# Optimization experiments

Measured on AMD Instinct MI355X. Metric: run time of the kernel, lower is better.

Reference implementation:

```python
import jax, jax.numpy as jnp
import numpy as np

B, N, IN_DIM = 16, 2048, 64
DIM, HEADS, DEPTH, K, NCLS = 512, 8, 4, 256, 2
DH = DIM // HEADS
EPS = 1e-5


def layernorm(h, s, b):
    mu = jnp.mean(h, axis=-1, keepdims=True)
    var = jnp.mean(jnp.square(h - mu), axis=-1, keepdims=True)
    return (h - mu) * jax.lax.rsqrt(var + EPS) * s + b


def setup_inputs() -> dict:
    key = jax.random.key(0)
    ks = jax.random.split(key, 20)
    w = 0.02
    L = DEPTH
    return {
        "x": jax.random.normal(ks[0], (B, N, IN_DIM), jnp.float32),
        "emb_w": jax.random.normal(ks[1], (IN_DIM, DIM), jnp.float32) * w,
        "emb_b": jnp.zeros((DIM,), jnp.float32),
        "pos": jax.random.normal(ks[2], (1, N, DIM), jnp.float32) * w,
        "ln1_s": jnp.ones((L, DIM), jnp.float32),
        "ln1_b": jnp.zeros((L, DIM), jnp.float32),
        "wq": jax.random.normal(ks[3], (L, DIM, DIM), jnp.float32) * w,
        "wk": jax.random.normal(ks[4], (L, DIM, DIM), jnp.float32) * w,
        "wv": jax.random.normal(ks[5], (L, DIM, DIM), jnp.float32) * w,
        "pk": jax.random.normal(ks[6], (L, N, K), jnp.float32) * (1.0 / np.sqrt(N)),
        "pv": jax.random.normal(ks[7], (L, N, K), jnp.float32) * (1.0 / np.sqrt(N)),
        "wo": jax.random.normal(ks[8], (L, DIM, DIM), jnp.float32) * w,
        "wo_b": jnp.zeros((L, DIM), jnp.float32),
        "ln2_s": jnp.ones((L, DIM), jnp.float32),
        "ln2_b": jnp.zeros((L, DIM), jnp.float32),
        "w1": jax.random.normal(ks[9], (L, DIM, 4 * DIM), jnp.float32) * w,
        "b1": jnp.zeros((L, 4 * DIM), jnp.float32),
        "w2": jax.random.normal(ks[10], (L, 4 * DIM, DIM), jnp.float32) * w,
        "b2": jnp.zeros((L, DIM), jnp.float32),
        "fc_w": jax.random.normal(ks[11], (DIM, NCLS), jnp.float32) * w,
        "fc_b": jnp.zeros((NCLS,), jnp.float32),
    }


def reference(x, emb_w, emb_b, pos, ln1_s, ln1_b, wq, wk, wv, pk, pv, wo, wo_b,
              ln2_s, ln2_b, w1, b1, w2, b2, fc_w, fc_b):
    scale = DH ** -0.5
    h = x @ emb_w + emb_b + pos  # [B,N,DIM]
    for i in range(DEPTH):
        # Linformer self-attention (PreNorm + residual)
        z = layernorm(h, ln1_s[i], ln1_b[i])
        q = (z @ wq[i]).reshape(B, N, HEADS, DH)
        k = z @ wk[i]  # [B,N,DIM]
        v = z @ wv[i]
        # low-rank projection along sequence: [B,N,DIM] x [N,K] -> [B,K,DIM]
        kp = jnp.einsum('bnd,nk->bkd', k, pk[i]).reshape(B, K, HEADS, DH)
        vp = jnp.einsum('bnd,nk->bkd', v, pv[i]).reshape(B, K, HEADS, DH)
        dots = jnp.einsum('bnhd,bkhd->bhnk', q, kp) * scale
        attn = jax.nn.softmax(dots, axis=-1)
        out = jnp.einsum('bhnk,bkhd->bnhd', attn, vp).reshape(B, N, DIM)
        h = h + out @ wo[i] + wo_b[i]
        # FeedForward (PreNorm + residual)
        z = layernorm(h, ln2_s[i], ln2_b[i])
        h = h + jax.nn.gelu(z @ w1[i] + b1[i]) @ w2[i] + b2[i]
    pooled = jnp.mean(h, axis=1)  # [B,DIM]
    return pooled @ fc_w + fc_b  # [B,NCLS]
```

## Files before the change

### kernel.cpp

```cpp
#include <hip/hip_runtime.h>
#include <math.h>

#define B_    16
#define N_    2048
#define INDIM 64
#define DIM_  512
#define HEADS 8
#define DEPTH 4
#define KLIN  256
#define NCLS  2
#define DH    64
#define EPSF  1e-5f

typedef __attribute__((ext_vector_type(8))) short short8v;
typedef __attribute__((ext_vector_type(4))) short short4v;
typedef __attribute__((ext_vector_type(4))) float f32x4;

#define SBAR() __builtin_amdgcn_sched_barrier(0)

__device__ __forceinline__ short f2bf(float f) {
  unsigned u = __float_as_uint(f);
  u += 0x7FFFu + ((u >> 16) & 1u);
  return (short)(u >> 16);
}

__device__ __forceinline__ float wave_sum(float v) {
  #pragma unroll
  for (int o = 32; o > 0; o >>= 1) v += __shfl_xor(v, o);
  return v;
}

__device__ __forceinline__ float gelu_tanh(float x) {
  float u = x * (1.5957691216057308f + 0.07135481627f * x * x);
  return x / (1.f + __expf(-u));
}

__device__ __forceinline__ void gl_lds16(const short* g, short* l) {
  __builtin_amdgcn_global_load_lds(
      (const __attribute__((address_space(1))) unsigned int*)g,
      (__attribute__((address_space(3))) unsigned int*)l, 16, 0, 0);
}

__global__ __launch_bounds__(256) void tconv_k(const float* __restrict__ src,
                                               short* __restrict__ dst, int R,
                                               int C, long long sSrc,
                                               long long sDst) {
  __shared__ float tile[32][33];
  int c0 = blockIdx.x * 32, r0 = blockIdx.y * 32;
  src += (long long)blockIdx.z * sSrc;
  dst += (long long)blockIdx.z * sDst;
  int tx = threadIdx.x & 31, ty = threadIdx.x >> 5;
  #pragma unroll
  for (int rr = 0; rr < 4; ++rr)
    tile[ty + rr * 8][tx] = src[(long long)(r0 + ty + rr * 8) * C + c0 + tx];
  __syncthreads();
  #pragma unroll
  for (int rr = 0; rr < 4; ++rr) {
    int c = ty + rr * 8;
    dst[(long long)(c0 + c) * R + r0 + tx] = f2bf(tile[tx][c]);
  }
}

__global__ __launch_bounds__(256) void cconv_k(const float* __restrict__ src,
                                               short* __restrict__ dst,
                                               int n8) {
  int i = blockIdx.x * 256 + threadIdx.x;
  if (i < n8) {
    const float* s = src + (long long)i * 8;
    float4 a = *(const float4*)s, c = *(const float4*)(s + 4);
    short8v o = {f2bf(a.x), f2bf(a.y), f2bf(a.z), f2bf(a.w),
                 f2bf(c.x), f2bf(c.y), f2bf(c.z), f2bf(c.w)};
    *(short8v*)(dst + (long long)i * 8) = o;
  }
}

__global__ __launch_bounds__(256) void tpose_k(const short* __restrict__ src,
                                               short* __restrict__ dst, int R,
                                               int C, long long sSrc,
                                               long long sDst) {
  __shared__ __align__(16) short tile[64][72];
  int c0 = blockIdx.x * 64, r0 = blockIdx.y * 64;
  src += (long long)blockIdx.z * sSrc;
  dst += (long long)blockIdx.z * sDst;
  int t = threadIdx.x;
  #pragma unroll
  for (int rep = 0; rep < 2; ++rep) {
    int row = rep * 32 + (t >> 3), c8 = (t & 7) * 8;
    *(short8v*)&tile[row][c8] =
        *(const short8v*)(src + (long long)(r0 + row) * C + c0 + c8);
  }
  __syncthreads();
  #pragma unroll
  for (int rep = 0; rep < 2; ++rep) {
    int c = rep * 32 + (t >> 3), r8 = (t & 7) * 8;
    short8v o;
    #pragma unroll
    for (int j = 0; j < 8; ++j) o[j] = tile[r8 + j][c];
    *(short8v*)(dst + (long long)(c0 + c) * R + r0 + r8) = o;
  }
}

__global__ __launch_bounds__(256) void ln_k(const float* __restrict__ h,
                                            const float* __restrict__ s,
                                            const float* __restrict__ b,
                                            short* __restrict__ z) {
  int lane = threadIdx.x & 63;
  long long row = ((long long)blockIdx.x << 2) + (threadIdx.x >> 6);
  const float* hr = h + row * DIM_ + lane * 8;
  float4 a = *(const float4*)hr;
  float4 c = *(const float4*)(hr + 4);
  float sum = a.x + a.y + a.z + a.w + c.x + c.y + c.z + c.w;
  sum = wave_sum(sum);
  float mu = sum * (1.f / DIM_);
  float d[8] = {a.x - mu, a.y - mu, a.z - mu, a.w - mu,
                c.x - mu, c.y - mu, c.z - mu, c.w - mu};
  float vs = 0.f;
  #pragma unroll
  for (int i = 0; i < 8; ++i) vs += d[i] * d[i];
  vs = wave_sum(vs);
  float rstd = rsqrtf(vs * (1.f / DIM_) + EPSF);
  const float* sp = s + lane * 8;
  const float* bp = b + lane * 8;
  float4 s0 = *(const float4*)sp, s1 = *(const float4*)(sp + 4);
  float4 b0 = *(const float4*)bp, b1 = *(const float4*)(bp + 4);
  float o[8];
  o[0] = d[0] * rstd * s0.x + b0.x; o[1] = d[1] * rstd * s0.y + b0.y;
  o[2] = d[2] * rstd * s0.z + b0.z; o[3] = d[3] * rstd * s0.w + b0.w;
  o[4] = d[4] * rstd * s1.x + b1.x; o[5] = d[5] * rstd * s1.y + b1.y;
  o[6] = d[6] * rstd * s1.z + b1.z; o[7] = d[7] * rstd * s1.w + b1.w;
  short8v ov = {f2bf(o[0]), f2bf(o[1]), f2bf(o[2]), f2bf(o[3]),
                f2bf(o[4]), f2bf(o[5]), f2bf(o[6]), f2bf(o[7])};
  *(short8v*)(z + row * DIM_ + lane * 8) = ov;
}

template <int OUTBF, int BM, int BN>
__global__ __launch_bounds__(256) void gemm_bf(
    const short* __restrict__ A, const short* __restrict__ Bsrc,
    const float* __restrict__ bias, const float* __restrict__ resid,
    void* __restrict__ Cv, int M, int N, int K, int lda, int ldb, int ldc,
    long long sAb, long long sBb, long long sCb, int dualThresh,
    long long dualOff, int epi, int resMod) {
  constexpr int MT = BM / 32;
  constexpr int NT = BN / 32;
  constexpr int NLD = BM / 32 + BN / 32;
  int zz = blockIdx.z;
  A += (long long)zz * sAb;
  Bsrc += (long long)zz * sBb;
  int bm = blockIdx.y * BM, bn = blockIdx.x * BN;
  if (dualThresh && bm >= dualThresh) Bsrc += dualOff;
  int t = threadIdx.x;
  __shared__ __align__(16) short Alds[2][BM * 64];
  __shared__ __align__(16) short Blds[2][BN * 64];
  int lane = t & 63, wid = t >> 6;
  int lr = lane & 15, q = lane >> 4;
  int wm = (wid >> 1) * (BM / 2), wn = (wid & 1) * (BN / 2);
  int rl = lane >> 3;
  int cs = (lane & 7) ^ rl;
  f32x4 acc[MT][NT] = {};

  auto stage = [&](int buf, int k0) {
    #pragma unroll
    for (int i = 0; i < BM / 32; ++i) {
      int rb = i * 32 + wid * 8;
      gl_lds16(A + (long long)(bm + rb + rl) * lda + k0 + cs * 8,
               &Alds[buf][rb * 64]);
    }
    #pragma unroll
    for (int i = 0; i < BN / 32; ++i) {
      int rb = i * 32 + wid * 8;
      gl_lds16(Bsrc + (long long)(bn + rb + rl) * ldb + k0 + cs * 8,
               &Blds[buf][rb * 64]);
    }
  };

  stage(0, 0);
  int cur = 0;
  for (int k0 = 0; k0 < K; k0 += 64, cur ^= 1) {
    if (k0 + 64 < K) {
      stage(cur ^ 1, k0 + 64);
      SBAR();
      asm volatile("s_waitcnt vmcnt(%0)" ::"n"(NLD) : "memory");
    } else {
      SBAR();
      asm volatile("s_waitcnt vmcnt(0)" ::: "memory");
    }
    __builtin_amdgcn_s_barrier();
    SBAR();
    #pragma unroll
    for (int kk2 = 0; kk2 < 2; ++kk2) {
      short8v af[MT], bfr[NT];
      #pragma unroll
      for (int mi = 0; mi < MT; ++mi)
        af[mi] = *(const short8v*)&Alds[cur][(wm + mi * 16 + lr) * 64 +
                                             (((kk2 << 2) | q) ^ (lr & 7)) * 8];
      #pragma unroll
      for (int ni = 0; ni < NT; ++ni)
        bfr[ni] = *(const short8v*)&Blds[cur][(wn + ni * 16 + lr) * 64 +
                                              (((kk2 << 2) | q) ^ (lr & 7)) * 8];
      #pragma unroll
      for (int mi = 0; mi < MT; ++mi)
        #pragma unroll
        for (int ni = 0; ni < NT; ++ni)
          acc[mi][ni] = __builtin_amdgcn_mfma_f32_16x16x32_bf16(
              bfr[ni], af[mi], acc[mi][ni], 0, 0, 0);
    }
    SBAR();
    __builtin_amdgcn_s_barrier();
  }

  #pragma unroll
  for (int mi = 0; mi < MT; ++mi) {
    int m = bm + wm + mi * 16 + lr;
    int rm = (epi == 2 && resMod) ? (m % resMod) : m;
    #pragma unroll
    for (int ni = 0; ni < NT; ++ni) {
      int nb = bn + wn + ni * 16 + q * 4;
      f32x4 v = acc[mi][ni];
      if (epi >= 1) {
        float4 bb = *(const float4*)(bias + nb);
        v[0] += bb.x; v[1] += bb.y; v[2] += bb.z; v[3] += bb.w;
      }
      if (epi == 2) {
        float4 rr = *(const float4*)(resid + (long long)rm * ldc + nb);
        v[0] += rr.x; v[1] += rr.y; v[2] += rr.z; v[3] += rr.w;
      } else if (epi == 3) {
        v[0] = gelu_tanh(v[0]); v[1] = gelu_tanh(v[1]);
        v[2] = gelu_tanh(v[2]); v[3] = gelu_tanh(v[3]);
      }
      long long base = (long long)zz * sCb + (long long)m * ldc + nb;
      if (OUTBF) {
        short4v o = {f2bf(v[0]), f2bf(v[1]), f2bf(v[2]), f2bf(v[3])};
        *(short4v*)((short*)Cv + base) = o;
      } else {
        *(float4*)((float*)Cv + base) = make_float4(v[0], v[1], v[2], v[3]);
      }
    }
  }
}

template <int OUTBF, int BM, int BN, int EPI>
__global__ __launch_bounds__(512, 2) void gemm8(
    const short* __restrict__ A, const short* __restrict__ Bt,
    const float* __restrict__ bias, const float* __restrict__ resid,
    void* __restrict__ Cv, int M, int N, int K, long long sAb, long long sBb,
    long long sCb, int dualThresh, long long dualOff) {
  constexpr int MH = BM / 64;
  constexpr int WCOL = BN / 4;
  constexpr int NT = WCOL / 16;
  constexpr int NTH = NT / 2;
  constexpr int LB = BN / 128;
  constexpr int LA = BM / 128;
  __shared__ __align__(16) short Alds[2][BM * 64];
  __shared__ __align__(16) short Blds[2][BN * 64];
  const int tid = threadIdx.x;
  const int lane = tid & 63, wid = tid >> 6;
  const int lr = lane & 15, q = lane >> 4;
  const int wm = (wid >> 2) * (BM / 2), wn = (wid & 3) * WCOL;
  const int rl = lane >> 3, cs = (lane & 7) ^ rl;
  const int zz = blockIdx.z;
  A += (long long)zz * sAb;
  Bt += (long long)zz * sBb;
  const int nwg = gridDim.x * gridDim.y;
  int bid = blockIdx.y * gridDim.x + blockIdx.x;
  const int nx8 = nwg >> 3, r8 = nwg & 7, xcd = bid & 7, loc = bid >> 3;
  int swz = (xcd < r8 ? xcd * (nx8 + 1) : r8 * (nx8 + 1) + (xcd - r8) * nx8)
            + loc;
  const int bm = (swz / gridDim.x) * BM, bn = (swz % gridDim.x) * BN;
  if (dualThresh && bm >= dualThresh) Bt += dualOff;
  const short* Ag = A + (long long)bm * K + cs * 8;
  const short* Bg = Bt + (long long)bn * K + cs * 8;
  f32x4 acc[2 * MH][NT] = {};

  auto stageA = [&](int slot, int h, int k0) {
    #pragma unroll
    for (int j = 0; j < LA; ++j) {
      int rb = h * (BM / 2) + j * 64 + wid * 8;
      gl_lds16(Ag + (long long)(rb + rl) * K + k0, &Alds[slot][rb * 64]);
    }
  };
  auto stageB = [&](int slot, int h, int k0) {
    #pragma unroll
    for (int j = 0; j < LB; ++j) {
      int rb = h * (BN / 2) + j * 64 + wid * 8;
      gl_lds16(Bg + (long long)(rb + rl) * K + k0, &Blds[slot][rb * 64]);
    }
  };
  auto rd = [&](const short* Ls, int row, int kk) -> short8v {
    return *(const short8v*)&Ls[row * 64 + ((((kk << 2) | q) ^ (lr & 7)) << 3)];
  };
  auto mfma4 = [&](short8v (&af)[MH][2], short8v (&bf)[NTH][2], int mo,
                   int no) {
    #pragma unroll
    for (int mi = 0; mi < MH; ++mi)
      #pragma unroll
      for (int ni = 0; ni < NTH; ++ni)
        #pragma unroll
        for (int kk = 0; kk < 2; ++kk)
          acc[mo + mi][no + ni] = __builtin_amdgcn_mfma_f32_16x16x32_bf16(
              bf[ni][kk], af[mi][kk], acc[mo + mi][no + ni], 0, 0, 0);
  };

  const int T = K >> 6;
  stageA(0, 0, 0); stageA(0, 1, 0); stageB(0, 0, 0); stageB(0, 1, 0);
  if (T > 1) {
    stageA(1, 0, 64);
    SBAR();
    asm volatile("s_waitcnt vmcnt(%0)" ::"n"(LA) : "memory");
  } else {
    SBAR();
    asm volatile("s_waitcnt vmcnt(0)" ::: "memory");
  }
  __builtin_amdgcn_s_barrier();

  for (int tt = 0; tt < T; ++tt) {
    const int s = tt & 1, ns = s ^ 1;
    const int kn = (tt + 1) << 6, kn2 = (tt + 2) << 6;
    const short* Als = Alds[s];
    const short* Bls = Blds[s];
    short8v af0[MH][2], af1[MH][2], bf0[NTH][2], bf1[NTH][2];
    SBAR();
    #pragma unroll
    for (int mi = 0; mi < MH; ++mi)
      #pragma unroll
      for (int kk = 0; kk < 2; ++kk)
        af0[mi][kk] = rd(Als, wm + mi * 16 + lr, kk);
    #pragma unroll
    for (int ni = 0; ni < NTH; ++ni)
      #pragma unroll
      for (int kk = 0; kk < 2; ++kk)
        bf0[ni][kk] = rd(Bls, wn + ni * 16 + lr, kk);
    if (tt + 1 < T) stageA(ns, 1, kn);
    if (BN == 256) asm volatile("s_waitcnt lgkmcnt(8)" ::: "memory");
    SBAR();
    __builtin_amdgcn_s_barrier();
    asm volatile("s_waitcnt lgkmcnt(0)" ::: "memory");
    SBAR();
    __builtin_amdgcn_s_setprio(1);
    mfma4(af0, bf0, 0, 0);
    __builtin_amdgcn_s_setprio(0);
    SBAR();
    __builtin_amdgcn_s_barrier();
    SBAR();
    #pragma unroll
    for (int ni = 0; ni < NTH; ++ni)
      #pragma unroll
      for (int kk = 0; kk < 2; ++kk)
        bf1[ni][kk] = rd(Bls, wn + (NTH + ni) * 16 + lr, kk);
    SBAR();
    __builtin_amdgcn_s_barrier();
    asm volatile("s_waitcnt lgkmcnt(0)" ::: "memory");
    SBAR();
    __builtin_amdgcn_s_setprio(1);
    mfma4(af0, bf1, 0, NTH);
    __builtin_amdgcn_s_setprio(0);
    SBAR();
    __builtin_amdgcn_s_barrier();
    SBAR();
    #pragma unroll
    for (int mi = 0; mi < MH; ++mi)
      #pragma unroll
      for (int kk = 0; kk < 2; ++kk)
        af1[mi][kk] = rd(Als, wm + MH * 16 + mi * 16 + lr, kk);
    if (tt + 1 < T) { stageB(ns, 0, kn); stageB(ns, 1, kn); }
    SBAR();
    __builtin_amdgcn_s_barrier();
    asm volatile("s_waitcnt lgkmcnt(0)" ::: "memory");
    SBAR();
    __builtin_amdgcn_s_setprio(1);
    mfma4(af1, bf0, MH, 0);
    __builtin_amdgcn_s_setprio(0);
    SBAR();
    __builtin_amdgcn_s_barrier();
    SBAR();
    if (tt + 2 < T) stageA(s, 0, kn2);
    SBAR();
    __builtin_amdgcn_s_barrier();
    __builtin_amdgcn_s_setprio(1);
    mfma4(af1, bf1, MH, NTH);
    __builtin_amdgcn_s_setprio(0);
    if (tt + 2 < T) {
      SBAR();
      asm volatile("s_waitcnt vmcnt(%0)" ::"n"(LA) : "memory");
    } else if (tt + 1 < T) {
      SBAR();
      asm volatile("s_waitcnt vmcnt(0)" ::: "memory");
    }
    SBAR();
    __builtin_amdgcn_s_barrier();
  }

  #pragma unroll
  for (int mi = 0; mi < 2 * MH; ++mi) {
    int m = bm + wm + mi * 16 + lr;
    #pragma unroll
    for (int nj = 0; nj < NT; ++nj) {
      int nb = bn + wn + nj * 16 + q * 4;
      f32x4 v = acc[mi][nj];
      if (EPI >= 1) {
        float4 bb = *(const float4*)(bias + nb);
        v[0] += bb.x; v[1] += bb.y; v[2] += bb.z; v[3] += bb.w;
      }
      if (EPI == 2) {
        float4 rr = *(const float4*)(resid + (long long)m * N + nb);
        v[0] += rr.x; v[1] += rr.y; v[2] += rr.z; v[3] += rr.w;
      } else if (EPI == 3) {
        v[0] = gelu_tanh(v[0]); v[1] = gelu_tanh(v[1]);
        v[2] = gelu_tanh(v[2]); v[3] = gelu_tanh(v[3]);
      }
      long long base = (long long)zz * sCb + (long long)m * N + nb;
      if (OUTBF) {
        short4v o = {f2bf(v[0]), f2bf(v[1]), f2bf(v[2]), f2bf(v[3])};
        *(short4v*)((short*)Cv + base) = o;
      } else {
        *(float4*)((float*)Cv + base) = make_float4(v[0], v[1], v[2], v[3]);
      }
    }
  }
}

template <int OUTBF, int BM, int BN, int EPI>
__global__ __launch_bounds__(512, 2) void gemm8m(
    const short* __restrict__ A, const short* __restrict__ Bt,
    const float* __restrict__ bias, const float* __restrict__ resid,
    void* __restrict__ Cv, int M, int N, int K, long long sAb, long long sBb,
    long long sCb, int dualThresh, long long dualOff) {
  constexpr int MH = BM / 64;
  constexpr int WCOL = BN / 4;
  constexpr int NT = WCOL / 16;
  constexpr int NTH = NT / 2;
  constexpr int LB = BN / 128;
  constexpr int LA = BM / 128;
  __shared__ __align__(16) short Alds[2][BM * 64];
  __shared__ __align__(16) short Blds[2][BN * 64];
  const int tid = threadIdx.x;
  const int lane = tid & 63, wid = tid >> 6;
  const int lr = lane & 15, q = lane >> 4;
  const int wm = (wid >> 2) * (BM / 2), wn = (wid & 3) * WCOL;
  const int rl = lane >> 3, cs = (lane & 7) ^ rl;
  const int zz = blockIdx.z;
  A += (long long)zz * sAb;
  Bt += (long long)zz * sBb;
  const int nwg = gridDim.x * gridDim.y;
  int bid = blockIdx.y * gridDim.x + blockIdx.x;
  const int nx8 = nwg >> 3, r8 = nwg & 7, xcd = bid & 7, loc = bid >> 3;
  int swz = (xcd < r8 ? xcd * (nx8 + 1) : r8 * (nx8 + 1) + (xcd - r8) * nx8)
            + loc;
  const int bm = (swz / gridDim.x) * BM, bn = (swz % gridDim.x) * BN;
  if (dualThresh && bm >= dualThresh) Bt += dualOff;
  const short* Ag = A + (long long)bm * K + cs * 8;
  const short* Bg = Bt + (long long)bn * K + cs * 8;
  f32x4 acc[2 * MH][NT] = {};

  auto stageA = [&](int slot, int h, int k0) {
    #pragma unroll
    for (int j = 0; j < LA; ++j) {
      int rb = h * (BM / 2) + j * 64 + wid * 8;
      gl_lds16(Ag + (long long)(rb + rl) * K + k0, &Alds[slot][rb * 64]);
    }
  };
  auto stageB = [&](int slot, int h, int k0) {
    #pragma unroll
    for (int j = 0; j < LB; ++j) {
      int rb = h * (BN / 2) + j * 64 + wid * 8;
      gl_lds16(Bg + (long long)(rb + rl) * K + k0, &Blds[slot][rb * 64]);
    }
  };
  auto rd = [&](const short* Ls, int row, int kk) -> short8v {
    return *(const short8v*)&Ls[row * 64 + ((((kk << 2) | q) ^ (lr & 7)) << 3)];
  };
  auto mfma4 = [&](short8v (&af)[MH][2], short8v (&bf)[NTH][2], int mo,
                   int no) {
    #pragma unroll
    for (int mi = 0; mi < MH; ++mi)
      #pragma unroll
      for (int ni = 0; ni < NTH; ++ni)
        #pragma unroll
        for (int kk = 0; kk < 2; ++kk)
          acc[mo + mi][no + ni] = __builtin_amdgcn_mfma_f32_16x16x32_bf16(
              bf[ni][kk], af[mi][kk], acc[mo + mi][no + ni], 0, 0, 0);
  };

  const int T = K >> 6;
  stageA(0, 0, 0); stageA(0, 1, 0); stageB(0, 0, 0); stageB(0, 1, 0);
  if (T > 1) {
    stageA(1, 0, 64);
    SBAR();
    asm volatile("s_waitcnt vmcnt(%0)" ::"n"(LA) : "memory");
  } else {
    SBAR();
    asm volatile("s_waitcnt vmcnt(0)" ::: "memory");
  }
  __builtin_amdgcn_s_barrier();

  for (int tt = 0; tt < T; ++tt) {
    const int s = tt & 1, ns = s ^ 1;
    const int kn = (tt + 1) << 6, kn2 = (tt + 2) << 6;
    const short* Als = Alds[s];
    const short* Bls = Blds[s];
    short8v af0[MH][2], af1[MH][2], bf0[NTH][2], bf1[NTH][2];
    SBAR();
    #pragma unroll
    for (int mi = 0; mi < MH; ++mi)
      #pragma unroll
      for (int kk = 0; kk < 2; ++kk)
        af0[mi][kk] = rd(Als, wm + mi * 16 + lr, kk);
    #pragma unroll
    for (int ni = 0; ni < NTH; ++ni)
      #pragma unroll
      for (int kk = 0; kk < 2; ++kk) {
        bf0[ni][kk] = rd(Bls, wn + ni * 16 + lr, kk);
        bf1[ni][kk] = rd(Bls, wn + (NTH + ni) * 16 + lr, kk);
      }
    if (tt + 1 < T) {
      stageA(ns, 1, kn);
      stageB(ns, 0, kn);
      stageB(ns, 1, kn);
    }
    SBAR();
    __builtin_amdgcn_s_barrier();
    asm volatile("s_waitcnt lgkmcnt(0)" ::: "memory");
    SBAR();
    __builtin_amdgcn_s_setprio(1);
    mfma4(af0, bf0, 0, 0);
    mfma4(af0, bf1, 0, NTH);
    __builtin_amdgcn_s_setprio(0);
    SBAR();
    __builtin_amdgcn_s_barrier();
    SBAR();
    #pragma unroll
    for (int mi = 0; mi < MH; ++mi)
      #pragma unroll
      for (int kk = 0; kk < 2; ++kk)
        af1[mi][kk] = rd(Als, wm + MH * 16 + mi * 16 + lr, kk);
    if (tt + 2 < T) stageA(s, 0, kn2);
    SBAR();
    __builtin_amdgcn_s_barrier();
    asm volatile("s_waitcnt lgkmcnt(0)" ::: "memory");
    SBAR();
    __builtin_amdgcn_s_setprio(1);
    mfma4(af1, bf0, MH, 0);
    mfma4(af1, bf1, MH, NTH);
    __builtin_amdgcn_s_setprio(0);
    if (tt + 2 < T) {
      SBAR();
      asm volatile("s_waitcnt vmcnt(%0)" ::"n"(LA) : "memory");
    } else if (tt + 1 < T) {
      SBAR();
      asm volatile("s_waitcnt vmcnt(0)" ::: "memory");
    }
    SBAR();
    __builtin_amdgcn_s_barrier();
  }

  #pragma unroll
  for (int mi = 0; mi < 2 * MH; ++mi) {
    int m = bm + wm + mi * 16 + lr;
    #pragma unroll
    for (int nj = 0; nj < NT; ++nj) {
      int nb = bn + wn + nj * 16 + q * 4;
      f32x4 v = acc[mi][nj];
      if (EPI >= 1) {
        float4 bb = *(const float4*)(bias + nb);
        v[0] += bb.x; v[1] += bb.y; v[2] += bb.z; v[3] += bb.w;
      }
      if (EPI == 2) {
        float4 rr = *(const float4*)(resid + (long long)m * N + nb);
        v[0] += rr.x; v[1] += rr.y; v[2] += rr.z; v[3] += rr.w;
      } else if (EPI == 3) {
        v[0] = gelu_tanh(v[0]); v[1] = gelu_tanh(v[1]);
        v[2] = gelu_tanh(v[2]); v[3] = gelu_tanh(v[3]);
      }
      long long base = (long long)zz * sCb + (long long)m * N + nb;
      if (OUTBF) {
        short4v o = {f2bf(v[0]), f2bf(v[1]), f2bf(v[2]), f2bf(v[3])};
        *(short4v*)((short*)Cv + base) = o;
      } else {
        *(float4*)((float*)Cv + base) = make_float4(v[0], v[1], v[2], v[3]);
      }
    }
  }
}

__global__ __launch_bounds__(256) void attn_k(short* __restrict__ qc,
                                              const short* __restrict__ kvp,
                                              const short* __restrict__ vt,
                                              float scale) {
  int n0 = blockIdx.x * 64, hh = blockIdx.y, b = blockIdx.z;
  int t = threadIdx.x;
  int lane = t & 63, w = t >> 6;
  int lr = lane & 15, qd = lane >> 4;

  __shared__ __align__(16) short Qlds[64][72];
  __shared__ __align__(16) short Kbuf[256 * 72];
  __shared__ __align__(16) short Vt[64][264];
  auto Klds = (short(*)[72])Kbuf;
  auto Plds = (short(*)[264])Kbuf;

  short* qptr = qc + (long long)b * N_ * DIM_ + hh * DH;
  const short* kptr = kvp + (long long)b * 2 * KLIN * DIM_ + hh * DH;
  const short* vtp = vt + (long long)b * DIM_ * KLIN + (long long)hh * DH * KLIN;

  #pragma unroll
  for (int rep = 0; rep < 2; ++rep) {
    int L = rep * 256 + t, row = L >> 3, c8 = (L & 7) << 3;
    *(short8v*)&Qlds[row][c8] =
        *(const short8v*)(qptr + (long long)(n0 + row) * DIM_ + c8);
  }
  #pragma unroll
  for (int rep = 0; rep < 8; ++rep) {
    int L = rep * 256 + t, row = L >> 3, c8 = (L & 7) << 3;
    *(short8v*)&Klds[row][c8] =
        *(const short8v*)(kptr + (long long)row * DIM_ + c8);
  }
  #pragma unroll
  for (int rep = 0; rep < 8; ++rep) {
    int L = rep * 256 + t, row = L >> 5, c8 = (L & 31) << 3;
    *(short8v*)&Vt[row][c8] =
        *(const short8v*)(vtp + (long long)row * KLIN + c8);
  }
  __syncthreads();

  short8v qa0 = *(const short8v*)&Qlds[16 * w + lr][qd * 8];
  short8v qa1 = *(const short8v*)&Qlds[16 * w + lr][32 + qd * 8];
  f32x4 sacc[16];
  #pragma unroll
  for (int nt = 0; nt < 16; ++nt) {
    short8v b0 = *(const short8v*)&Klds[nt * 16 + lr][qd * 8];
    short8v b1 = *(const short8v*)&Klds[nt * 16 + lr][32 + qd * 8];
    f32x4 acc = {};
    acc = __builtin_amdgcn_mfma_f32_16x16x32_bf16(b0, qa0, acc, 0, 0, 0);
    acc = __builtin_amdgcn_mfma_f32_16x16x32_bf16(b1, qa1, acc, 0, 0, 0);
    sacc[nt] = acc;
  }

  float mx = -1e30f;
  #pragma unroll
  for (int nt = 0; nt < 16; ++nt)
    #pragma unroll
    for (int r = 0; r < 4; ++r) mx = fmaxf(mx, sacc[nt][r]);
  mx = fmaxf(mx, __shfl_xor(mx, 16));
  mx = fmaxf(mx, __shfl_xor(mx, 32));
  float rs = 0.f;
  #pragma unroll
  for (int nt = 0; nt < 16; ++nt)
    #pragma unroll
    for (int r = 0; r < 4; ++r) {
      float e = __expf((sacc[nt][r] - mx) * scale);
      sacc[nt][r] = e;
      rs += e;
    }
  rs += __shfl_xor(rs, 16);
  rs += __shfl_xor(rs, 32);
  float inv = 1.f / rs;

  __syncthreads();
  #pragma unroll
  for (int nt = 0; nt < 16; ++nt) {
    short4v p = {f2bf(sacc[nt][0] * inv), f2bf(sacc[nt][1] * inv),
                 f2bf(sacc[nt][2] * inv), f2bf(sacc[nt][3] * inv)};
    *(short4v*)&Plds[16 * w + lr][nt * 16 + qd * 4] = p;
  }
  __syncthreads();

  f32x4 out[4] = {};
  #pragma unroll
  for (int k0 = 0; k0 < 8; ++k0) {
    short8v ap = *(const short8v*)&Plds[16 * w + lr][k0 * 32 + qd * 8];
    #pragma unroll
    for (int n2 = 0; n2 < 4; ++n2) {
      short8v bv = *(const short8v*)&Vt[n2 * 16 + lr][k0 * 32 + qd * 8];
      out[n2] =
          __builtin_amdgcn_mfma_f32_16x16x32_bf16(bv, ap, out[n2], 0, 0, 0);
    }
  }

  long long rowoff = (long long)(n0 + 16 * w + lr) * DIM_;
  #pragma unroll
  for (int n2 = 0; n2 < 4; ++n2) {
    short4v o = {f2bf(out[n2][0]), f2bf(out[n2][1]), f2bf(out[n2][2]),
                 f2bf(out[n2][3])};
    *(short4v*)(qptr + rowoff + n2 * 16 + qd * 4) = o;
  }
}

__global__ __launch_bounds__(256) void pool1_k(const float* __restrict__ h,
                                               float* __restrict__ partial) {
  int stripe = blockIdx.x, b = blockIdx.y;
  int c4 = (threadIdx.x & 127) * 4, half = threadIdx.x >> 7;
  const float* base =
      h + ((long long)b * N_ + stripe * 128 + half * 64) * DIM_ + c4;
  float4 acc = {0.f, 0.f, 0.f, 0.f};
  for (int r = 0; r < 64; ++r) {
    float4 v = *(const float4*)(base + (long long)r * DIM_);
    acc.x += v.x; acc.y += v.y; acc.z += v.z; acc.w += v.w;
  }
  __shared__ float red[512];
  if (half == 1) *(float4*)&red[c4] = acc;
  __syncthreads();
  if (half == 0) {
    float4 o = *(const float4*)&red[c4];
    o.x += acc.x; o.y += acc.y; o.z += acc.z; o.w += acc.w;
    *(float4*)&partial[((long long)b * 16 + stripe) * DIM_ + c4] = o;
  }
}
__global__ __launch_bounds__(256) void pool2_k(const float* __restrict__ partial,
                                               float* __restrict__ pooled) {
  int b = blockIdx.x;
  for (int c = threadIdx.x; c < DIM_; c += 256) {
    float s = 0.f;
    for (int k = 0; k < 16; ++k) s += partial[((long long)b * 16 + k) * DIM_ + c];
    pooled[b * DIM_ + c] = s * (1.f / N_);
  }
}

__global__ __launch_bounds__(64) void fc_k(const float* __restrict__ pooled,
                                           const float* __restrict__ fc_w,
                                           const float* __restrict__ fc_b,
                                           float* __restrict__ out) {
  int t = threadIdx.x;
  if (t < B_ * NCLS) {
    int b = t >> 1, c = t & 1;
    float s = fc_b[c];
    for (int d = 0; d < DIM_; ++d)
      s += pooled[b * DIM_ + d] * fc_w[d * NCLS + c];
    out[t] = s;
  }
}

extern "C" void kernel_launch(void* const* d_in, const int* in_sizes, int n_in,
                              void* d_out, int out_size, void* d_ws,
                              size_t ws_size, hipStream_t stream) {
  const float* x     = (const float*)d_in[0];
  const float* emb_w = (const float*)d_in[1];
  const float* emb_b = (const float*)d_in[2];
  const float* pos   = (const float*)d_in[3];
  const float* ln1_s = (const float*)d_in[4];
  const float* ln1_b = (const float*)d_in[5];
  const float* wq    = (const float*)d_in[6];
  const float* wk    = (const float*)d_in[7];
  const float* wv    = (const float*)d_in[8];
  const float* pk    = (const float*)d_in[9];
  const float* pv    = (const float*)d_in[10];
  const float* wo    = (const float*)d_in[11];
  const float* wo_b  = (const float*)d_in[12];
  const float* ln2_s = (const float*)d_in[13];
  const float* ln2_b = (const float*)d_in[14];
  const float* w1    = (const float*)d_in[15];
  const float* b1    = (const float*)d_in[16];
  const float* w2    = (const float*)d_in[17];
  const float* b2    = (const float*)d_in[18];
  const float* fc_w  = (const float*)d_in[19];
  const float* fc_b  = (const float*)d_in[20];
  float* out = (float*)d_out;

  const bool big = ws_size >= (size_t)230 * 1024 * 1024;
  const int acb = big ? 16 : 8;
  const long long acrows = (long long)acb * N_;
  const int frows = big ? 16384 : 8192;

  char* P = (char*)d_ws;
  float* h = (float*)P;            P += (long long)B_ * N_ * DIM_ * 4;
  short* zc = (short*)P;           P += acrows * DIM_ * 2;
  short* qc = (short*)P;           P += acrows * DIM_ * 2;
  short* ffnmid = zc;
  short* zcT = (short*)P;          P += acrows * DIM_ * 2;
  short* zln = zcT;
  short* zp = (short*)P;           P += (long long)acb * 2 * KLIN * DIM_ * 2;
  short* kvp = (short*)P;          P += (long long)acb * 2 * KLIN * DIM_ * 2;
  short* vt = zp;
  short* wq_t  = (short*)P;  P += (long long)DEPTH * DIM_ * DIM_ * 2;
  short* wkv_t = (short*)P;  P += (long long)DEPTH * 2 * DIM_ * DIM_ * 2;
  short* wo_t  = (short*)P;  P += (long long)DEPTH * DIM_ * DIM_ * 2;
  short* w1_t  = (short*)P;  P += (long long)DEPTH * 4 * DIM_ * DIM_ * 2;
  short* w2_t  = (short*)P;  P += (long long)DEPTH * 4 * DIM_ * DIM_ * 2;
  short* pkv_t = (short*)P;  P += (long long)DEPTH * 2 * KLIN * N_ * 2;
  short* emb_wt = (short*)P; P += (long long)DIM_ * INDIM * 2;
  short* x_bf  = (short*)P;  P += (long long)B_ * N_ * INDIM * 2;
  float* partial = (float*)P; P += (long long)B_ * 16 * DIM_ * 4;
  float* pooled  = (float*)P;

  const float scale = 0.125f;
  const long long WQS = (long long)DIM_ * DIM_;
  const long long KVS = (long long)2 * KLIN * DIM_;

  auto tconv = [&](const float* s, short* d, int R, int C, long long ss,
                   long long sd, int b) {
    hipLaunchKernelGGL(tconv_k, dim3(C / 32, R / 32, b), dim3(256), 0, stream,
                       s, d, R, C, ss, sd);
  };
  tconv(wq, wq_t, DIM_, DIM_, WQS, WQS, DEPTH);
  tconv(wk, wkv_t, DIM_, DIM_, WQS, 2 * WQS, DEPTH);
  tconv(wv, wkv_t + WQS, DIM_, DIM_, WQS, 2 * WQS, DEPTH);
  tconv(wo, wo_t, DIM_, DIM_, WQS, WQS, DEPTH);
  tconv(w1, w1_t, DIM_, 4 * DIM_, 4 * WQS, 4 * WQS, DEPTH);
  tconv(w2, w2_t, 4 * DIM_, DIM_, 4 * WQS, 4 * WQS, DEPTH);
  tconv(pk, pkv_t, N_, KLIN, (long long)N_ * KLIN, (long long)2 * KLIN * N_, DEPTH);
  tconv(pv, pkv_t + (long long)KLIN * N_, N_, KLIN, (long long)N_ * KLIN,
        (long long)2 * KLIN * N_, DEPTH);
  tconv(emb_w, emb_wt, INDIM, DIM_, 0, 0, 1);
  hipLaunchKernelGGL(cconv_k, dim3((B_ * N_ * INDIM / 8 + 255) / 256),
                     dim3(256), 0, stream, x, x_bf, B_ * N_ * INDIM / 8);

  hipLaunchKernelGGL((gemm_bf<0, 128, 128>), dim3(DIM_ / 128, B_ * N_ / 128, 1),
                     dim3(256), 0, stream, x_bf, emb_wt, emb_b, pos, (void*)h,
                     B_ * N_, DIM_, INDIM, INDIM, INDIM, DIM_, 0LL, 0LL, 0LL,
                     0, 0LL, 2, N_);

  for (int i = 0; i < DEPTH; ++i) {
    const short* wq_i  = wq_t + i * WQS;
    const short* wkv_i = wkv_t + i * 2 * WQS;
    const short* wo_i  = wo_t + i * WQS;
    const short* w1_i  = w1_t + (long long)i * 4 * WQS;
    const short* w2_i  = w2_t + (long long)i * 4 * WQS;
    const short* pkv_i = pkv_t + (long long)i * 2 * KLIN * N_;

    for (int c = 0; c < B_ / acb; ++c) {
      float* hc = h + (long long)c * acrows * DIM_;
      hipLaunchKernelGGL(ln_k, dim3(acrows / 4), dim3(256), 0, stream, hc,
                         ln1_s + i * DIM_, ln1_b + i * DIM_, zc);
      hipLaunchKernelGGL(tpose_k, dim3(DIM_ / 64, N_ / 64, acb), dim3(256), 0,
                         stream, zc, zcT, N_, DIM_, (long long)N_ * DIM_,
                         (long long)DIM_ * N_);
      hipLaunchKernelGGL((gemm8<1, 256, 256, 0>),
                         dim3(DIM_ / 256, (int)(acrows / 256), 1), dim3(512), 0,
                         stream, zc, wq_i, nullptr, nullptr, (void*)qc,
                         (int)acrows, DIM_, DIM_, 0LL, 0LL, 0LL, 0, 0LL);
      hipLaunchKernelGGL((gemm_bf<1, 64, 128>), dim3(DIM_ / 128, 512 / 64, acb),
                         dim3(256), 0, stream, pkv_i, zcT, nullptr, nullptr,
                         (void*)zp, 512, DIM_, N_, N_, N_, DIM_, 0LL,
                         (long long)DIM_ * N_, KVS, 0, 0LL, 0, 0);
      hipLaunchKernelGGL((gemm_bf<1, 64, 128>), dim3(DIM_ / 128, 512 / 64, acb),
                         dim3(256), 0, stream, zp, wkv_i, nullptr, nullptr,
                         (void*)kvp, 512, DIM_, DIM_, DIM_, DIM_, DIM_, KVS,
                         0LL, KVS, KLIN, (long long)WQS, 0, 0);
      hipLaunchKernelGGL(tpose_k, dim3(DIM_ / 64, KLIN / 64, acb), dim3(256), 0,
                         stream, kvp + (long long)KLIN * DIM_, vt, KLIN, DIM_,
                         KVS, (long long)DIM_ * KLIN);
      hipLaunchKernelGGL(attn_k, dim3(N_ / 64, HEADS, acb), dim3(256), 0,
                         stream, qc, kvp, vt, scale);
      hipLaunchKernelGGL((gemm8<0, 256, 256, 2>),
                         dim3(DIM_ / 256, (int)(acrows / 256), 1), dim3(512), 0,
                         stream, qc, wo_i, wo_b + i * DIM_, hc, (void*)hc,
                         (int)acrows, DIM_, DIM_, 0LL, 0LL, 0LL, 0, 0LL);
    }

    for (int r0 = 0; r0 < B_ * N_; r0 += frows) {
      float* hr = h + (long long)r0 * DIM_;
      hipLaunchKernelGGL(ln_k, dim3(frows / 4), dim3(256), 0, stream, hr,
                         ln2_s + i * DIM_, ln2_b + i * DIM_, zln);
      hipLaunchKernelGGL((gemm8m<1, 128, 128, 3>),
                         dim3(4 * DIM_ / 128, frows / 128, 1), dim3(512), 0,
                         stream, zln, w1_i, b1 + (long long)i * 4 * DIM_,
                         nullptr, (void*)ffnmid, frows, 4 * DIM_, DIM_, 0LL,
                         0LL, 0LL, 0, 0LL);
      hipLaunchKernelGGL((gemm8m<0, 128, 128, 2>),
                         dim3(DIM_ / 128, frows / 128, 1), dim3(512), 0,
                         stream, ffnmid, w2_i, b2 + (long long)i * DIM_, hr,
                         (void*)hr, frows, DIM_, 4 * DIM_, 0LL, 0LL, 0LL, 0,
                         0LL);
    }
  }

  hipLaunchKernelGGL(pool1_k, dim3(16, B_), dim3(256), 0, stream, h, partial);
  hipLaunchKernelGGL(pool2_k, dim3(B_), dim3(256), 0, stream, partial, pooled);
  hipLaunchKernelGGL(fc_k, dim3(1), dim3(64), 0, stream, pooled, fc_w, fc_b,
                     out);
}
```

Before: 1.838 ms.

## Store residual stream in bf16 instead of fp32

The residual activation buffer h is switched from fp32 to bf16. The embedding GEMM, the attention output projection and the FFN down-projection now write bf16. LayerNorm, the residual epilogues and pooling read bf16 and convert back to fp32. This halves the memory traffic on the residual stream across all layers, but rounds the residual to bf16 after every block, which risks accumulated precision loss.

```diff
diff --git a/kernel.cpp b/kernel.cpp
--- a/kernel.cpp
+++ b/kernel.cpp
@@ -23,6 +23,9 @@
   u += 0x7FFFu + ((u >> 16) & 1u);
   return (short)(u >> 16);
 }
+__device__ __forceinline__ float bf2f(short s) {
+  return __uint_as_float((unsigned)(unsigned short)s << 16);
+}
 
 __device__ __forceinline__ float wave_sum(float v) {
   #pragma unroll
@@ -100,20 +103,25 @@
   }
 }
 
-__global__ __launch_bounds__(256) void ln_k(const float* __restrict__ h,
+__global__ __launch_bounds__(256) void ln_k(const short* __restrict__ h,
                                             const float* __restrict__ s,
                                             const float* __restrict__ b,
                                             short* __restrict__ z) {
   int lane = threadIdx.x & 63;
   long long row = ((long long)blockIdx.x << 2) + (threadIdx.x >> 6);
-  const float* hr = h + row * DIM_ + lane * 8;
-  float4 a = *(const float4*)hr;
-  float4 c = *(const float4*)(hr + 4);
-  float sum = a.x + a.y + a.z + a.w + c.x + c.y + c.z + c.w;
+  const short* hr = h + row * DIM_ + lane * 8;
+  short8v hv = *(const short8v*)hr;
+  float x[8];
+  #pragma unroll
+  for (int i = 0; i < 8; ++i) x[i] = bf2f(hv[i]);
+  float sum = 0.f;
+  #pragma unroll
+  for (int i = 0; i < 8; ++i) sum += x[i];
   sum = wave_sum(sum);
   float mu = sum * (1.f / DIM_);
-  float d[8] = {a.x - mu, a.y - mu, a.z - mu, a.w - mu,
-                c.x - mu, c.y - mu, c.z - mu, c.w - mu};
+  float d[8];
+  #pragma unroll
+  for (int i = 0; i < 8; ++i) d[i] = x[i] - mu;
   float vs = 0.f;
   #pragma unroll
   for (int i = 0; i < 8; ++i) vs += d[i] * d[i];
@@ -401,8 +409,10 @@
         v[0] += bb.x; v[1] += bb.y; v[2] += bb.z; v[3] += bb.w;
       }
       if (EPI == 2) {
-        float4 rr = *(const float4*)(resid + (long long)m * N + nb);
-        v[0] += rr.x; v[1] += rr.y; v[2] += rr.z; v[3] += rr.w;
+        const short* rp = (const short*)resid;
+        short4v rr = *(const short4v*)(rp + (long long)m * N + nb);
+        v[0] += bf2f(rr[0]); v[1] += bf2f(rr[1]);
+        v[2] += bf2f(rr[2]); v[3] += bf2f(rr[3]);
       } else if (EPI == 3) {
         v[0] = gelu_tanh(v[0]); v[1] = gelu_tanh(v[1]);
         v[2] = gelu_tanh(v[2]); v[3] = gelu_tanh(v[3]);
@@ -564,8 +574,10 @@
         v[0] += bb.x; v[1] += bb.y; v[2] += bb.z; v[3] += bb.w;
       }
       if (EPI == 2) {
-        float4 rr = *(const float4*)(resid + (long long)m * N + nb);
-        v[0] += rr.x; v[1] += rr.y; v[2] += rr.z; v[3] += rr.w;
+        const short* rp = (const short*)resid;
+        short4v rr = *(const short4v*)(rp + (long long)m * N + nb);
+        v[0] += bf2f(rr[0]); v[1] += bf2f(rr[1]);
+        v[2] += bf2f(rr[2]); v[3] += bf2f(rr[3]);
       } else if (EPI == 3) {
         v[0] = gelu_tanh(v[0]); v[1] = gelu_tanh(v[1]);
         v[2] = gelu_tanh(v[2]); v[3] = gelu_tanh(v[3]);
@@ -683,24 +695,33 @@
   }
 }
 
-__global__ __launch_bounds__(256) void pool1_k(const float* __restrict__ h,
+__global__ __launch_bounds__(256) void pool1_k(const short* __restrict__ h,
                                                float* __restrict__ partial) {
   int stripe = blockIdx.x, b = blockIdx.y;
-  int c4 = (threadIdx.x & 127) * 4, half = threadIdx.x >> 7;
-  const float* base =
-      h + ((long long)b * N_ + stripe * 128 + half * 64) * DIM_ + c4;
-  float4 acc = {0.f, 0.f, 0.f, 0.f};
-  for (int r = 0; r < 64; ++r) {
-    float4 v = *(const float4*)(base + (long long)r * DIM_);
-    acc.x += v.x; acc.y += v.y; acc.z += v.z; acc.w += v.w;
-  }
-  __shared__ float red[512];
-  if (half == 1) *(float4*)&red[c4] = acc;
+  int c8 = (threadIdx.x & 63) * 8, grp = threadIdx.x >> 6;
+  const short* base =
+      h + ((long long)b * N_ + stripe * 128 + grp * 32) * DIM_ + c8;
+  float acc[8] = {};
+  for (int r = 0; r < 32; ++r) {
+    short8v v = *(const short8v*)(base + (long long)r * DIM_);
+    #pragma unroll
+    for (int i = 0; i < 8; ++i) acc[i] += bf2f(v[i]);
+  }
+  __shared__ float red[3][512];
+  if (grp) {
+    *(float4*)&red[grp - 1][c8] = make_float4(acc[0], acc[1], acc[2], acc[3]);
+    *(float4*)&red[grp - 1][c8 + 4] =
+        make_float4(acc[4], acc[5], acc[6], acc[7]);
+  }
   __syncthreads();
-  if (half == 0) {
-    float4 o = *(const float4*)&red[c4];
-    o.x += acc.x; o.y += acc.y; o.z += acc.z; o.w += acc.w;
-    *(float4*)&partial[((long long)b * 16 + stripe) * DIM_ + c4] = o;
+  if (grp == 0) {
+    float o[8];
+    #pragma unroll
+    for (int i = 0; i < 8; ++i)
+      o[i] = acc[i] + red[0][c8 + i] + red[1][c8 + i] + red[2][c8 + i];
+    float* pp = &partial[((long long)b * 16 + stripe) * DIM_ + c8];
+    *(float4*)pp = make_float4(o[0], o[1], o[2], o[3]);
+    *(float4*)(pp + 4) = make_float4(o[4], o[5], o[6], o[7]);
   }
 }
 __global__ __launch_bounds__(256) void pool2_k(const float* __restrict__ partial,
@@ -759,7 +780,7 @@
   const int frows = big ? 16384 : 8192;
 
   char* P = (char*)d_ws;
-  float* h = (float*)P;            P += (long long)B_ * N_ * DIM_ * 4;
+  short* h = (short*)P;            P += (long long)B_ * N_ * DIM_ * 2;
   short* zc = (short*)P;           P += acrows * DIM_ * 2;
   short* qc = (short*)P;           P += acrows * DIM_ * 2;
   short* ffnmid = zc;
@@ -801,7 +822,7 @@
   hipLaunchKernelGGL(cconv_k, dim3((B_ * N_ * INDIM / 8 + 255) / 256),
                      dim3(256), 0, stream, x, x_bf, B_ * N_ * INDIM / 8);
 
-  hipLaunchKernelGGL((gemm_bf<0, 128, 128>), dim3(DIM_ / 128, B_ * N_ / 128, 1),
+  hipLaunchKernelGGL((gemm_bf<1, 128, 128>), dim3(DIM_ / 128, B_ * N_ / 128, 1),
                      dim3(256), 0, stream, x_bf, emb_wt, emb_b, pos, (void*)h,
                      B_ * N_, DIM_, INDIM, INDIM, INDIM, DIM_, 0LL, 0LL, 0LL,
                      0, 0LL, 2, N_);
@@ -815,7 +836,7 @@
     const short* pkv_i = pkv_t + (long long)i * 2 * KLIN * N_;
 
     for (int c = 0; c < B_ / acb; ++c) {
-      float* hc = h + (long long)c * acrows * DIM_;
+      short* hc = h + (long long)c * acrows * DIM_;
       hipLaunchKernelGGL(ln_k, dim3(acrows / 4), dim3(256), 0, stream, hc,
                          ln1_s + i * DIM_, ln1_b + i * DIM_, zc);
       hipLaunchKernelGGL(tpose_k, dim3(DIM_ / 64, N_ / 64, acb), dim3(256), 0,
@@ -838,14 +859,15 @@
                          KVS, (long long)DIM_ * KLIN);
       hipLaunchKernelGGL(attn_k, dim3(N_ / 64, HEADS, acb), dim3(256), 0,
                          stream, qc, kvp, vt, scale);
-      hipLaunchKernelGGL((gemm8<0, 256, 256, 2>),
+      hipLaunchKernelGGL((gemm8<1, 256, 256, 2>),
                          dim3(DIM_ / 256, (int)(acrows / 256), 1), dim3(512), 0,
-                         stream, qc, wo_i, wo_b + i * DIM_, hc, (void*)hc,
-                         (int)acrows, DIM_, DIM_, 0LL, 0LL, 0LL, 0, 0LL);
+                         stream, qc, wo_i, wo_b + i * DIM_,
+                         (const float*)hc, (void*)hc, (int)acrows, DIM_, DIM_,
+                         0LL, 0LL, 0LL, 0, 0LL);
     }
 
     for (int r0 = 0; r0 < B_ * N_; r0 += frows) {
-      float* hr = h + (long long)r0 * DIM_;
+      short* hr = h + (long long)r0 * DIM_;
       hipLaunchKernelGGL(ln_k, dim3(frows / 4), dim3(256), 0, stream, hr,
                          ln2_s + i * DIM_, ln2_b + i * DIM_, zln);
       hipLaunchKernelGGL((gemm8m<1, 128, 128, 3>),
@@ -853,11 +875,11 @@
                          stream, zln, w1_i, b1 + (long long)i * 4 * DIM_,
                          nullptr, (void*)ffnmid, frows, 4 * DIM_, DIM_, 0LL,
                          0LL, 0LL, 0, 0LL);
-      hipLaunchKernelGGL((gemm8m<0, 128, 128, 2>),
+      hipLaunchKernelGGL((gemm8m<1, 128, 128, 2>),
                          dim3(DIM_ / 128, frows / 128, 1), dim3(512), 0,
-                         stream, ffnmid, w2_i, b2 + (long long)i * DIM_, hr,
-                         (void*)hr, frows, DIM_, 4 * DIM_, 0LL, 0LL, 0LL, 0,
-                         0LL);
+                         stream, ffnmid, w2_i, b2 + (long long)i * DIM_,
+                         (const float*)hr, (void*)hr, frows, DIM_, 4 * DIM_,
+                         0LL, 0LL, 0LL, 0, 0LL);
     }
   }
 
```

Result: no change. 1.806 ms (-1.8%).
